# Optimization experiments

Hardware: AMD Instinct MI355X
Metric: run time of the kernel (lower is better)

Reference implementation:

```python
import jax, jax.numpy as jnp
import numpy as np

E = 512   # embed_size
H = 8     # num_heads
D = E // H
N = 4
T = 2048


def quantize(x, b, e):
    # fake-quant: scale by 2^e, clamp to signed b-bit range, floor, dequant
    s = jnp.exp2(e)
    lo = -jnp.exp2(b - 1.0)
    hi = jnp.exp2(b - 1.0) - 1.0
    return jnp.floor(jnp.clip(x / s, lo, hi)) * s


def setup_inputs() -> dict:
    key = jax.random.key(0)
    ks = jax.random.split(key, 8)
    f = lambda k, shape: jax.random.normal(k, shape, dtype=jnp.float32)
    w = 1.0 / np.sqrt(E)  # ~ torch Linear init scale
    return {
        "values": f(ks[0], (N, T, E)),
        "keys": f(ks[1], (N, T, E)),
        "query": f(ks[2], (N, T, E)),
        "Wq": f(ks[3], (E, E)) * w, "bq": jnp.zeros((E,), jnp.float32),
        "Wk": f(ks[4], (E, E)) * w, "bk": jnp.zeros((E,), jnp.float32),
        "Wv": f(ks[5], (E, E)) * w, "bv": jnp.zeros((E,), jnp.float32),
        "Wo": f(ks[6], (E, E)) * w, "bo": jnp.zeros((E,), jnp.float32),
        "b_param": jnp.float32(8.0),
        "e_param": jnp.float32(0.0),
    }


def reference(values, keys, query, Wq, bq, Wk, bk, Wv, bv, Wo, bo, b_param, e_param):
    n, t, emb = query.shape
    d = emb // H
    # linear projections (torch Linear: x @ W^T + b), split heads -> [N,H,T,D]
    q = (query @ Wq.T + bq).reshape(n, t, H, d).transpose(0, 2, 1, 3)
    k = (keys @ Wk.T + bk).reshape(n, t, H, d).transpose(0, 2, 1, 3)
    v = (values @ Wv.T + bv).reshape(n, t, H, d).transpose(0, 2, 1, 3)
    b = jnp.clip(b_param, 1.0, 8.0)
    q = quantize(q, b, e_param)
    k = quantize(k, b, e_param)
    v = quantize(v, b, e_param)
    # NOTE: source scales by sqrt(embed_size), not sqrt(head_dim)
    energy = jnp.einsum('nhqd,nhkd->nhqk', q, k) / jnp.sqrt(jnp.float32(emb))
    attn = jax.nn.softmax(energy, axis=-1)
    out = jnp.einsum('nhqk,nhkd->nhqd', attn, v)
    out = out.transpose(0, 2, 1, 3).reshape(n, t, emb)
    return out @ Wo.T + bo
```

## Files before the change

kernel.cpp:

```cpp
#include <hip/hip_runtime.h>
#include <hip/hip_bf16.h>
#include <hip/hip_fp16.h>
#include <cstdint>
#include <cstddef>


typedef __attribute__((ext_vector_type(8))) _Float16 f16x8;
typedef __attribute__((ext_vector_type(2))) __fp16 hf16x2;
typedef __attribute__((ext_vector_type(16))) float f32x16;
typedef __attribute__((ext_vector_type(4))) unsigned u32x4;
typedef unsigned short u16;

#define EL  4194304
#define WEL 262144

static __device__ __forceinline__ u16 f2h(float x) {
  _Float16 h = (_Float16)x;
  return __builtin_bit_cast(u16, h);
}
static __device__ __forceinline__ unsigned pkh2(float a, float b) {
  hf16x2 p = __builtin_amdgcn_cvt_pkrtz(a, b);
  return __builtin_bit_cast(unsigned, p);
}
static __device__ __forceinline__ void gl_lds16(const void* g, void* l) {
  __builtin_amdgcn_global_load_lds(
      (__attribute__((address_space(1))) void*)g,
      (__attribute__((address_space(3))) void*)l, 16, 0, 0);
}

struct PrepAllArgs { const float* src[7]; };

__global__ __launch_bounds__(256) void prep_all_kernel(PrepAllArgs a,
                                                       u16* __restrict__ dst)
{
  const int i = blockIdx.x * 256 + threadIdx.x;
  const float* src; int off;
  if (i < 3145728) {
    const int m = i >> 20; off = i & 1048575;
    src = (m == 0) ? a.src[0] : (m == 1) ? a.src[1] : a.src[2];
  } else {
    const int j = i - 3145728; const int w = j >> 16; off = j & 65535;
    src = (w == 0) ? a.src[3] : (w == 1) ? a.src[4]
        : (w == 2) ? a.src[5] : a.src[6];
  }
  const float4 v = ((const float4*)src)[off];
  ushort4 o;
  o.x = f2h(v.x); o.y = f2h(v.y); o.z = f2h(v.z); o.w = f2h(v.w);
  ((ushort4*)dst)[i] = o;
}

struct ProjArgs {
  const u16* X[3]; const u16* W[3]; const float* bias[3];
  u16* dst[3]; int trans[3];
};

__global__ __launch_bounds__(256, 3) void proj_kernel(ProjArgs args,
    const float* __restrict__ bparam, const float* __restrict__ eparam)
{
  __shared__ u16 sm[17408];
  u16* const As = sm;
  u16* const Bs = sm + 8192;

  const int z = blockIdx.z;
  const u16* __restrict__ X = args.X[z];
  const u16* __restrict__ W = args.W[z];
  const float* __restrict__ bias = args.bias[z];
  u16* __restrict__ dst = args.dst[z];
  const int mode = args.trans[z];

  const int tid  = threadIdx.x;
  const int lane = tid & 63;
  const int wave = tid >> 6;
  const int lam  = lane & 31;
  const int hl   = lane >> 5;
  const int wm   = wave & 1;
  const int wn   = wave >> 1;
  const int mbase = blockIdx.x * 128;
  const int nbase = blockIdx.y * 128;

  const int srow = tid >> 3;
  const int sj   = (tid & 7) ^ (srow & 7);
  const u16* gA = X + (size_t)(mbase + srow) * 512 + sj * 8;
  const u16* gB = W + (size_t)(nbase + srow) * 512 + sj * 8;

  int offA[2][4], offB[2][4];
#pragma unroll
  for (int f = 0; f < 2; ++f)
#pragma unroll
    for (int kk = 0; kk < 4; ++kk) {
      const int c = 2 * kk + hl;
      const int m = wm * 64 + f * 32 + lam;
      offA[f][kk] = m * 128 + ((c ^ (m & 7)) * 16);
      const int nn = wn * 64 + f * 32 + lam;
      offB[f][kk] = nn * 128 + ((c ^ (nn & 7)) * 16);
    }

  f32x16 acc[2][2];
#pragma unroll
  for (int a = 0; a < 2; ++a)
#pragma unroll
    for (int b = 0; b < 2; ++b)
#pragma unroll
      for (int i = 0; i < 16; ++i) acc[a][b][i] = 0.f;

  for (int kt = 0; kt < 512; kt += 64) {
    __syncthreads();
#pragma unroll
    for (int t = 0; t < 4; ++t) {
      gl_lds16(gA + kt + t * 32 * 512, (char*)As + tid * 16 + t * 4096);
      gl_lds16(gB + kt + t * 32 * 512, (char*)Bs + tid * 16 + t * 4096);
    }
    __syncthreads();

    f16x8 fA[2][4], fB[2][4];
#pragma unroll
    for (int f = 0; f < 2; ++f)
#pragma unroll
      for (int kk = 0; kk < 4; ++kk) {
        fA[f][kk] = *(const f16x8*)((const char*)As + offA[f][kk]);
        fB[f][kk] = *(const f16x8*)((const char*)Bs + offB[f][kk]);
      }
#pragma unroll
    for (int mf = 0; mf < 2; ++mf)
#pragma unroll
      for (int nf = 0; nf < 2; ++nf)
#pragma unroll
        for (int kk = 0; kk < 4; ++kk)
          acc[mf][nf] = __builtin_amdgcn_mfma_f32_32x32x16_f16(
              fA[mf][kk], fB[nf][kk], acc[mf][nf], 0, 0, 0);
  }

  const float bq   = fminf(fmaxf(bparam[0], 1.0f), 8.0f);
  const float e    = eparam[0];
  const float s    = exp2f(e);
  const float invs = exp2f(-e);
  const float qlo  = -exp2f(bq - 1.0f);
  const float qhi  = exp2f(bq - 1.0f) - 1.0f;
  const int nidx = mbase >> 11;
  const int tb   = mbase & 2047;
  const int hb   = nbase >> 6;

  if (mode == 0) {
    const float SCQ = (float)(1.4426950408889634 / 22.627416997969522);
#pragma unroll
    for (int mf = 0; mf < 2; ++mf)
#pragma unroll
      for (int nf = 0; nf < 2; ++nf)
#pragma unroll
        for (int reg = 0; reg < 16; ++reg) {
          int col = wn * 64 + nf * 32 + lam;
          int row = wm * 64 + mf * 32 + (reg & 3) + 8 * (reg >> 2) + 4 * hl;
          float v = acc[mf][nf][reg] + bias[nbase + col];
          float qv = floorf(fminf(fmaxf(v * invs, qlo), qhi)) * s;
          dst[((size_t)(nidx * 8 + hb + (col >> 6)) * 2048 + tb + row) * 64 +
              (col & 63)] = f2h(qv * SCQ);
        }
  } else if (mode == 1) {
#pragma unroll
    for (int mf = 0; mf < 2; ++mf)
#pragma unroll
      for (int nf = 0; nf < 2; ++nf)
#pragma unroll
        for (int reg = 0; reg < 16; ++reg) {
          int col = wn * 64 + nf * 32 + lam;
          int row = wm * 64 + mf * 32 + (reg & 3) + 8 * (reg >> 2) + 4 * hl;
          float v = acc[mf][nf][reg] + bias[nbase + col];
          float qv = floorf(fminf(fmaxf(v * invs, qlo), qhi)) * s;
          const int t = tb + row;
          const int d = col & 63;
          dst[(size_t)(nidx * 8 + hb + (col >> 6)) * 131072 +
              (t >> 5) * 2048 + (t & 31) * 64 + (((d >> 3) ^ (t & 7)) << 3) +
              (d & 7)] = f2h(qv);
        }
  } else {
    __syncthreads();
#pragma unroll
    for (int mf = 0; mf < 2; ++mf)
#pragma unroll
      for (int nf = 0; nf < 2; ++nf)
#pragma unroll
        for (int reg = 0; reg < 16; ++reg) {
          int col = wn * 64 + nf * 32 + lam;
          int row = wm * 64 + mf * 32 + (reg & 3) + 8 * (reg >> 2) + 4 * hl;
          float v = acc[mf][nf][reg] + bias[nbase + col];
          float qv = floorf(fminf(fmaxf(v * invs, qlo), qhi)) * s;
          sm[col * 136 + row] = f2h(qv);
        }
    __syncthreads();
    const int r = tid >> 1, half = tid & 1;
    const u16* sp = sm + r * 136 + half * 64;
    const int d  = r & 63;
    const int sb = d & 1;
    const int rx = (d >> 1) & 7;
    u16* const gp0 = dst + (size_t)(nidx * 8 + hb + (r >> 6)) * 131072 +
                     (d >> 1) * 64;
#pragma unroll
    for (int kb = 0; kb < 2; ++kb) {
      const int Bg = ((tb + half * 64) >> 5) + kb;
#pragma unroll
      for (int g = 0; g < 4; ++g) {
        const int qoff = (g & 1) * 4 + (g >> 1) * 16;
        const uint2 lo = *(const uint2*)(sp + kb * 32 + qoff);
        const uint2 hi = *(const uint2*)(sp + kb * 32 + qoff + 8);
        uint4 val; val.x = lo.x; val.y = lo.y; val.z = hi.x; val.w = hi.y;
        const int s2 = ((g << 1) | sb) ^ rx;
        *(uint4*)(gp0 + Bg * 2048 + s2 * 8) = val;
      }
    }
  }
}

__global__ __launch_bounds__(256, 4) void attn_kernel(
    const u16* __restrict__ qbuf, const u16* __restrict__ kbuf,
    const u16* __restrict__ vtbuf, u16* __restrict__ ctx)
{
  __shared__ u16 sm[17664];
  char* const smc = (char*)sm;

  const int tid  = threadIdx.x;
  const int wave = tid >> 6;
  const int lane = tid & 63;
  const int lam  = lane & 31;
  const int hl   = lane >> 5;
  const int kw   = wave & 1;
  const int qh   = wave >> 1;
  const int bid = blockIdx.x;
  const int wg  = (bid & 7) * 128 + (bid >> 3);
  const int qt = wg & 31;
  const int nh = wg >> 5;
  const int hd = nh & 7;
  const int n  = nh >> 3;
  const int qbase = qt * 64;

  const u16* Qp = qbuf + ((size_t)nh * 2048 + qbase + qh * 32) * 64;
  const u16* gK = kbuf  + (size_t)nh * 131072;
  const u16* gV = vtbuf + (size_t)nh * 131072;

  f16x8 qf[4];
#pragma unroll
  for (int dk = 0; dk < 4; ++dk)
    qf[dk] = *(const f16x8*)(Qp + lam * 64 + dk * 16 + hl * 8);
#pragma unroll
  for (int dk = 0; dk < 4; ++dk)
    asm volatile("" :: "v"(qf[dk]));

  auto stageK = [&](int tn, char* db) {
    const int e = tn * 4096 + tid * 8;
    gl_lds16(gK + e,        db + tid * 16);
    gl_lds16(gK + e + 2048, db + 4096 + tid * 16);
  };
  auto stageV = [&](int tn, char* db) {
    const int e = tn * 4096 + tid * 8;
    gl_lds16(gV + e,        db + tid * 16);
    gl_lds16(gV + e + 2048, db + 4096 + tid * 16);
  };

  int offK[4];
#pragma unroll
  for (int dk = 0; dk < 4; ++dk)
    offK[dk] = kw * 4096 + lam * 128 + (((2 * dk + hl) ^ (lam & 7)) << 4);
  int offV[2][2];
#pragma unroll
  for (int nf = 0; nf < 2; ++nf)
#pragma unroll
    for (int kkl = 0; kkl < 2; ++kkl) {
      const int R = nf * 16 + (lam >> 1);
      const int s2 = (((2 * kkl + hl) << 1) | (lam & 1)) ^ (R & 7);
      offV[nf][kkl] = 16384 + kw * 4096 + R * 128 + s2 * 16;
    }

  f32x16 Zc;
#pragma unroll
  for (int i = 0; i < 16; ++i) Zc[i] = 0.f;

  float l_acc = 0.f;
  f32x16 O[2];
#pragma unroll
  for (int b = 0; b < 2; ++b)
#pragma unroll
    for (int i = 0; i < 16; ++i) O[b][i] = 0.f;

  stageK(0, smc + 8192);
  stageV(0, smc + 16384);
  stageK(1, smc);
  asm volatile("s_waitcnt vmcnt(4)" ::: "memory");
  __builtin_amdgcn_s_barrier();
  f16x8 pf0, pf1;
  {
    f16x8 Kf[4];
#pragma unroll
    for (int dk = 0; dk < 4; ++dk)
      Kf[dk] = *(const f16x8*)(smc + 8192 + offK[dk]);
    f32x16 S;
    S = __builtin_amdgcn_mfma_f32_32x32x16_f16(Kf[0], qf[0], Zc, 0, 0, 0);
    S = __builtin_amdgcn_mfma_f32_32x32x16_f16(Kf[1], qf[1], S, 0, 0, 0);
    S = __builtin_amdgcn_mfma_f32_32x32x16_f16(Kf[2], qf[2], S, 0, 0, 0);
    S = __builtin_amdgcn_mfma_f32_32x32x16_f16(Kf[3], qf[3], S, 0, 0, 0);
    u32x4 fr[2];
#pragma unroll
    for (int gh = 0; gh < 4; ++gh) {
      float p0 = __builtin_amdgcn_exp2f(S[4 * gh + 0]);
      float p1 = __builtin_amdgcn_exp2f(S[4 * gh + 1]);
      float p2 = __builtin_amdgcn_exp2f(S[4 * gh + 2]);
      float p3 = __builtin_amdgcn_exp2f(S[4 * gh + 3]);
      l_acc += (p0 + p1) + (p2 + p3);
      fr[gh >> 1][(gh & 1) * 2 + 0] = pkh2(p0, p1);
      fr[gh >> 1][(gh & 1) * 2 + 1] = pkh2(p2, p3);
    }
    pf0 = __builtin_bit_cast(f16x8, fr[0]);
    pf1 = __builtin_bit_cast(f16x8, fr[1]);
  }

  for (int r = 0; r < 31; ++r) {
    asm volatile("s_waitcnt vmcnt(0)" ::: "memory");
    __builtin_amdgcn_s_barrier();
    __builtin_amdgcn_sched_barrier(0);

    const int pb = (r & 1) << 13;
    const int nb = pb ^ 8192;
    stageK((r + 2) & 31, smc + nb);
    stageV((r + 1) & 31, smc + 16384 + nb);

    f16x8 Vf[2][2];
#pragma unroll
    for (int nf = 0; nf < 2; ++nf)
#pragma unroll
      for (int kkl = 0; kkl < 2; ++kkl)
        Vf[nf][kkl] = *(const f16x8*)(smc + pb + offV[nf][kkl]);
    f16x8 Kf[4];
#pragma unroll
    for (int dk = 0; dk < 4; ++dk)
      Kf[dk] = *(const f16x8*)(smc + pb + offK[dk]);

    __builtin_amdgcn_s_setprio(1);
    O[0] = __builtin_amdgcn_mfma_f32_32x32x16_f16(pf0, Vf[0][0], O[0], 0, 0, 0);
    O[0] = __builtin_amdgcn_mfma_f32_32x32x16_f16(pf1, Vf[0][1], O[0], 0, 0, 0);
    O[1] = __builtin_amdgcn_mfma_f32_32x32x16_f16(pf0, Vf[1][0], O[1], 0, 0, 0);
    O[1] = __builtin_amdgcn_mfma_f32_32x32x16_f16(pf1, Vf[1][1], O[1], 0, 0, 0);
    f32x16 S;
    S = __builtin_amdgcn_mfma_f32_32x32x16_f16(Kf[0], qf[0], Zc, 0, 0, 0);
    S = __builtin_amdgcn_mfma_f32_32x32x16_f16(Kf[1], qf[1], S, 0, 0, 0);
    S = __builtin_amdgcn_mfma_f32_32x32x16_f16(Kf[2], qf[2], S, 0, 0, 0);
    S = __builtin_amdgcn_mfma_f32_32x32x16_f16(Kf[3], qf[3], S, 0, 0, 0);
    __builtin_amdgcn_s_setprio(0);

    u32x4 fr[2];
#pragma unroll
    for (int gh = 0; gh < 4; ++gh) {
      float p0 = __builtin_amdgcn_exp2f(S[4 * gh + 0]);
      float p1 = __builtin_amdgcn_exp2f(S[4 * gh + 1]);
      float p2 = __builtin_amdgcn_exp2f(S[4 * gh + 2]);
      float p3 = __builtin_amdgcn_exp2f(S[4 * gh + 3]);
      l_acc += (p0 + p1) + (p2 + p3);
      fr[gh >> 1][(gh & 1) * 2 + 0] = pkh2(p0, p1);
      fr[gh >> 1][(gh & 1) * 2 + 1] = pkh2(p2, p3);
    }
    pf0 = __builtin_bit_cast(f16x8, fr[0]);
    pf1 = __builtin_bit_cast(f16x8, fr[1]);
  }

  asm volatile("s_waitcnt vmcnt(0)" ::: "memory");
  __builtin_amdgcn_s_barrier();
  {
    f16x8 Vf[2][2];
#pragma unroll
    for (int nf = 0; nf < 2; ++nf)
#pragma unroll
      for (int kkl = 0; kkl < 2; ++kkl)
        Vf[nf][kkl] = *(const f16x8*)(smc + 8192 + offV[nf][kkl]);
    O[0] = __builtin_amdgcn_mfma_f32_32x32x16_f16(pf0, Vf[0][0], O[0], 0, 0, 0);
    O[0] = __builtin_amdgcn_mfma_f32_32x32x16_f16(pf1, Vf[0][1], O[0], 0, 0, 0);
    O[1] = __builtin_amdgcn_mfma_f32_32x32x16_f16(pf0, Vf[1][0], O[1], 0, 0, 0);
    O[1] = __builtin_amdgcn_mfma_f32_32x32x16_f16(pf1, Vf[1][1], O[1], 0, 0, 0);
  }

  l_acc += __shfl_xor(l_acc, 32);
  float* lred = (float*)(smc + 34816);
  if (hl == 0) lred[wave * 32 + lam] = l_acc;
  __syncthreads();

  float* Ow = (float*)(smc + wave * 8704);
#pragma unroll
  for (int nf = 0; nf < 2; ++nf)
#pragma unroll
    for (int r = 0; r < 16; ++r) {
      const int qrow = (r & 3) + 8 * (r >> 2) + 4 * hl;
      Ow[qrow * 68 + nf * 32 + lam] = O[nf][r];
    }
  __syncthreads();

  const int q  = tid >> 2;
  const int dc = (tid & 3) * 16;
  const int qh2 = q >> 5;
  float a[16];
  {
    const char* b0 = smc + (qh2 * 2) * 8704 + (q & 31) * 272 + dc * 4;
    const char* b1 = b0 + 8704;
#pragma unroll
    for (int j = 0; j < 4; ++j) {
      const float4 v0 = *(const float4*)(b0 + j * 16);
      const float4 v1 = *(const float4*)(b1 + j * 16);
      a[4 * j + 0] = v0.x + v1.x; a[4 * j + 1] = v0.y + v1.y;
      a[4 * j + 2] = v0.z + v1.z; a[4 * j + 3] = v0.w + v1.w;
    }
  }
  const float lsum = lred[qh2 * 64 + (q & 31)] + lred[qh2 * 64 + 32 + (q & 31)];
  const float rinv = 1.0f / lsum;
  unsigned outp[8];
#pragma unroll
  for (int i = 0; i < 8; ++i)
    outp[i] = pkh2(a[2 * i] * rinv, a[2 * i + 1] * rinv);
  u16* cp = ctx + ((size_t)n * 2048 + qbase + q) * 512 + hd * 64 + dc;
  *(uint4*)cp       = *(const uint4*)&outp[0];
  *(uint4*)(cp + 8) = *(const uint4*)&outp[4];
}

__global__ __launch_bounds__(256) void outproj_kernel(
    const u16* __restrict__ ctxb, const u16* __restrict__ Wof,
    const float* __restrict__ bias, float* __restrict__ out)
{
  __shared__ u16 sm[12288];
  u16* const As = sm;
  u16* const Bs = sm + 4096;

  const int tid  = threadIdx.x;
  const int lane = tid & 63;
  const int wave = tid >> 6;
  const int lam  = lane & 31;
  const int hl   = lane >> 5;
  const int wm   = wave & 1;
  const int wn   = wave >> 1;
  const int mbase = blockIdx.x * 64;
  const int nbase = blockIdx.y * 128;

  const int srow = tid >> 3;
  const int sj   = (tid & 7) ^ (srow & 7);
  const u16* gA = ctxb + (size_t)(mbase + srow) * 512 + sj * 8;
  const u16* gB = Wof  + (size_t)(nbase + srow) * 512 + sj * 8;

  int offA[4], offB[2][4];
#pragma unroll
  for (int kk = 0; kk < 4; ++kk) {
    const int c = 2 * kk + hl;
    const int m = wm * 32 + lam;
    offA[kk] = m * 128 + ((c ^ (m & 7)) * 16);
#pragma unroll
    for (int f = 0; f < 2; ++f) {
      const int nn = wn * 64 + f * 32 + lam;
      offB[f][kk] = nn * 128 + ((c ^ (nn & 7)) * 16);
    }
  }

  f32x16 acc[2];
#pragma unroll
  for (int a = 0; a < 2; ++a)
#pragma unroll
    for (int i = 0; i < 16; ++i) acc[a][i] = 0.f;

  for (int kt = 0; kt < 512; kt += 64) {
    __syncthreads();
#pragma unroll
    for (int t = 0; t < 2; ++t)
      gl_lds16(gA + kt + t * 32 * 512, (char*)As + tid * 16 + t * 4096);
#pragma unroll
    for (int t = 0; t < 4; ++t)
      gl_lds16(gB + kt + t * 32 * 512, (char*)Bs + tid * 16 + t * 4096);
    __syncthreads();

    f16x8 fA[4], fB[2][4];
#pragma unroll
    for (int kk = 0; kk < 4; ++kk) {
      fA[kk] = *(const f16x8*)((const char*)As + offA[kk]);
#pragma unroll
      for (int f = 0; f < 2; ++f)
        fB[f][kk] = *(const f16x8*)((const char*)Bs + offB[f][kk]);
    }
#pragma unroll
    for (int nf = 0; nf < 2; ++nf)
#pragma unroll
      for (int kk = 0; kk < 4; ++kk)
        acc[nf] = __builtin_amdgcn_mfma_f32_32x32x16_f16(
            fA[kk], fB[nf][kk], acc[nf], 0, 0, 0);
  }

#pragma unroll
  for (int nf = 0; nf < 2; ++nf)
#pragma unroll
    for (int reg = 0; reg < 16; ++reg) {
      int col = nbase + wn * 64 + nf * 32 + lam;
      int row = mbase + wm * 32 + (reg & 3) + 8 * (reg >> 2) + 4 * hl;
      out[(size_t)row * 512 + col] = acc[nf][reg] + bias[col];
    }
}

extern "C" void kernel_launch(void* const* d_in, const int* in_sizes, int n_in,
                              void* d_out, int out_size, void* d_ws, size_t ws_size,
                              hipStream_t stream) {
  (void)in_sizes; (void)n_in; (void)out_size; (void)ws_size;
  const float* values = (const float*)d_in[0];
  const float* keys   = (const float*)d_in[1];
  const float* query  = (const float*)d_in[2];
  const float* Wq = (const float*)d_in[3];  const float* bq = (const float*)d_in[4];
  const float* Wk = (const float*)d_in[5];  const float* bk = (const float*)d_in[6];
  const float* Wv = (const float*)d_in[7];  const float* bv = (const float*)d_in[8];
  const float* Wo = (const float*)d_in[9];  const float* bo = (const float*)d_in[10];
  const float* bp = (const float*)d_in[11]; const float* ep = (const float*)d_in[12];

  u16* ws    = (u16*)d_ws;
  u16* qbuf  = ws;
  u16* kbuf  = ws + (size_t)EL;
  u16* vtbuf = ws + (size_t)2 * EL;
  u16* ctx   = ws + (size_t)3 * EL;
  u16* xwf   = ws + (size_t)4 * EL;

  PrepAllArgs pa;
  pa.src[0] = query; pa.src[1] = keys; pa.src[2] = values;
  pa.src[3] = Wq; pa.src[4] = Wk; pa.src[5] = Wv; pa.src[6] = Wo;
  prep_all_kernel<<<13312, 256, 0, stream>>>(pa, xwf);

  const float* Bsrc[3] = {bq, bk, bv};
  u16* Dst[3] = {qbuf, kbuf, vtbuf};
  ProjArgs a;
  for (int m = 0; m < 3; ++m) {
    a.X[m] = xwf + (size_t)m * EL;
    a.W[m] = xwf + (size_t)3 * EL + (size_t)m * WEL;
    a.bias[m] = Bsrc[m]; a.dst[m] = Dst[m]; a.trans[m] = m;
  }
  proj_kernel<<<dim3(64, 4, 3), 256, 0, stream>>>(a, bp, ep);

  attn_kernel<<<dim3(1024), 256, 0, stream>>>(qbuf, kbuf, vtbuf, ctx);
  outproj_kernel<<<dim3(128, 4), 256, 0, stream>>>(
      ctx, xwf + (size_t)3 * EL + (size_t)3 * WEL, bo, (float*)d_out);
}
```

Baseline: 181.0 us.

## Stage Q/K projection epilogue through LDS and enlarge outproj tile to 128x128

The Q and K projection epilogues now write quantized fp16 results into shared memory first, then emit coalesced 16-byte row stores (with the XOR swizzle applied per 8-element chunk for K). This replaces scattered 2-byte global stores. The output projection kernel doubles its M tile to 128, giving each wave a 2x2 MFMA fragment grid, and sets a launch bound of 3 blocks per CU. The bigger tile improves operand reuse but halves the grid to 256 blocks and raises register and LDS use per block.

```diff
diff --git a/kernel.cpp b/kernel.cpp
--- a/kernel.cpp
+++ b/kernel.cpp
@@ -140,8 +140,10 @@
   const int tb   = mbase & 2047;
   const int hb   = nbase >> 6;
 
-  if (mode == 0) {
-    const float SCQ = (float)(1.4426950408889634 / 22.627416997969522);
+  if (mode != 2) {
+    const float SCQ = (mode == 0)
+        ? (float)(1.4426950408889634 / 22.627416997969522) : 1.0f;
+    __syncthreads();
 #pragma unroll
     for (int mf = 0; mf < 2; ++mf)
 #pragma unroll
@@ -152,26 +154,26 @@
           int row = wm * 64 + mf * 32 + (reg & 3) + 8 * (reg >> 2) + 4 * hl;
           float v = acc[mf][nf][reg] + bias[nbase + col];
           float qv = floorf(fminf(fmaxf(v * invs, qlo), qhi)) * s;
-          dst[((size_t)(nidx * 8 + hb + (col >> 6)) * 2048 + tb + row) * 64 +
-              (col & 63)] = f2h(qv * SCQ);
+          sm[row * 136 + col] = f2h(qv * SCQ);
         }
-  } else if (mode == 1) {
-#pragma unroll
-    for (int mf = 0; mf < 2; ++mf)
-#pragma unroll
-      for (int nf = 0; nf < 2; ++nf)
-#pragma unroll
-        for (int reg = 0; reg < 16; ++reg) {
-          int col = wn * 64 + nf * 32 + lam;
-          int row = wm * 64 + mf * 32 + (reg & 3) + 8 * (reg >> 2) + 4 * hl;
-          float v = acc[mf][nf][reg] + bias[nbase + col];
-          float qv = floorf(fminf(fmaxf(v * invs, qlo), qhi)) * s;
-          const int t = tb + row;
-          const int d = col & 63;
-          dst[(size_t)(nidx * 8 + hb + (col >> 6)) * 131072 +
-              (t >> 5) * 2048 + (t & 31) * 64 + (((d >> 3) ^ (t & 7)) << 3) +
-              (d & 7)] = f2h(qv);
-        }
+    __syncthreads();
+    const int r  = tid & 127;
+    const int hh = tid >> 7;
+    const u16* sp = sm + r * 136 + hh * 64;
+    const int t = tb + r;
+    if (mode == 0) {
+      u16* gp = dst + ((size_t)(nidx * 8 + hb + hh) * 2048 + t) * 64;
+#pragma unroll
+      for (int j = 0; j < 8; ++j)
+        *(uint4*)(gp + j * 8) = *(const uint4*)(sp + j * 8);
+    } else {
+      u16* gp = dst + (size_t)(nidx * 8 + hb + hh) * 131072 +
+                (t >> 5) * 2048 + (t & 31) * 64;
+      const int tx = t & 7;
+#pragma unroll
+      for (int j = 0; j < 8; ++j)
+        *(uint4*)(gp + ((j ^ tx) * 8)) = *(const uint4*)(sp + j * 8);
+    }
   } else {
     __syncthreads();
 #pragma unroll
@@ -415,13 +417,13 @@
   *(uint4*)(cp + 8) = *(const uint4*)&outp[4];
 }
 
-__global__ __launch_bounds__(256) void outproj_kernel(
+__global__ __launch_bounds__(256, 3) void outproj_kernel(
     const u16* __restrict__ ctxb, const u16* __restrict__ Wof,
     const float* __restrict__ bias, float* __restrict__ out)
 {
-  __shared__ u16 sm[12288];
+  __shared__ u16 sm[16384];
   u16* const As = sm;
-  u16* const Bs = sm + 4096;
+  u16* const Bs = sm + 8192;
 
   const int tid  = threadIdx.x;
   const int lane = tid & 63;
@@ -430,7 +432,7 @@
   const int hl   = lane >> 5;
   const int wm   = wave & 1;
   const int wn   = wave >> 1;
-  const int mbase = blockIdx.x * 64;
+  const int mbase = blockIdx.x * 128;
   const int nbase = blockIdx.y * 128;
 
   const int srow = tid >> 3;
@@ -438,59 +440,63 @@
   const u16* gA = ctxb + (size_t)(mbase + srow) * 512 + sj * 8;
   const u16* gB = Wof  + (size_t)(nbase + srow) * 512 + sj * 8;
 
-  int offA[4], offB[2][4];
-#pragma unroll
-  for (int kk = 0; kk < 4; ++kk) {
-    const int c = 2 * kk + hl;
-    const int m = wm * 32 + lam;
-    offA[kk] = m * 128 + ((c ^ (m & 7)) * 16);
-#pragma unroll
-    for (int f = 0; f < 2; ++f) {
+  int offA[2][4], offB[2][4];
+#pragma unroll
+  for (int f = 0; f < 2; ++f)
+#pragma unroll
+    for (int kk = 0; kk < 4; ++kk) {
+      const int c = 2 * kk + hl;
+      const int m = wm * 64 + f * 32 + lam;
+      offA[f][kk] = m * 128 + ((c ^ (m & 7)) * 16);
       const int nn = wn * 64 + f * 32 + lam;
       offB[f][kk] = nn * 128 + ((c ^ (nn & 7)) * 16);
     }
-  }
-
-  f32x16 acc[2];
+
+  f32x16 acc[2][2];
 #pragma unroll
   for (int a = 0; a < 2; ++a)
 #pragma unroll
-    for (int i = 0; i < 16; ++i) acc[a][i] = 0.f;
+    for (int b = 0; b < 2; ++b)
+#pragma unroll
+      for (int i = 0; i < 16; ++i) acc[a][b][i] = 0.f;
 
   for (int kt = 0; kt < 512; kt += 64) {
     __syncthreads();
 #pragma unroll
-    for (int t = 0; t < 2; ++t)
+    for (int t = 0; t < 4; ++t) {
       gl_lds16(gA + kt + t * 32 * 512, (char*)As + tid * 16 + t * 4096);
-#pragma unroll
-    for (int t = 0; t < 4; ++t)
       gl_lds16(gB + kt + t * 32 * 512, (char*)Bs + tid * 16 + t * 4096);
-    __syncthreads();
-
-    f16x8 fA[4], fB[2][4];
-#pragma unroll
-    for (int kk = 0; kk < 4; ++kk) {
-      fA[kk] = *(const f16x8*)((const char*)As + offA[kk]);
-#pragma unroll
-      for (int f = 0; f < 2; ++f)
+    }
+    __syncthreads();
+
+    f16x8 fA[2][4], fB[2][4];
+#pragma unroll
+    for (int f = 0; f < 2; ++f)
+#pragma unroll
+      for (int kk = 0; kk < 4; ++kk) {
+        fA[f][kk] = *(const f16x8*)((const char*)As + offA[f][kk]);
         fB[f][kk] = *(const f16x8*)((const char*)Bs + offB[f][kk]);
-    }
+      }
+#pragma unroll
+    for (int mf = 0; mf < 2; ++mf)
+#pragma unroll
+      for (int nf = 0; nf < 2; ++nf)
+#pragma unroll
+        for (int kk = 0; kk < 4; ++kk)
+          acc[mf][nf] = __builtin_amdgcn_mfma_f32_32x32x16_f16(
+              fA[mf][kk], fB[nf][kk], acc[mf][nf], 0, 0, 0);
+  }
+
+#pragma unroll
+  for (int mf = 0; mf < 2; ++mf)
 #pragma unroll
     for (int nf = 0; nf < 2; ++nf)
 #pragma unroll
-      for (int kk = 0; kk < 4; ++kk)
-        acc[nf] = __builtin_amdgcn_mfma_f32_32x32x16_f16(
-            fA[kk], fB[nf][kk], acc[nf], 0, 0, 0);
-  }
-
-#pragma unroll
-  for (int nf = 0; nf < 2; ++nf)
-#pragma unroll
-    for (int reg = 0; reg < 16; ++reg) {
-      int col = nbase + wn * 64 + nf * 32 + lam;
-      int row = mbase + wm * 32 + (reg & 3) + 8 * (reg >> 2) + 4 * hl;
-      out[(size_t)row * 512 + col] = acc[nf][reg] + bias[col];
-    }
+      for (int reg = 0; reg < 16; ++reg) {
+        int col = nbase + wn * 64 + nf * 32 + lam;
+        int row = mbase + wm * 64 + mf * 32 + (reg & 3) + 8 * (reg >> 2) + 4 * hl;
+        out[(size_t)row * 512 + col] = acc[mf][nf][reg] + bias[col];
+      }
 }
 
 extern "C" void kernel_launch(void* const* d_in, const int* in_sizes, int n_in,
@@ -529,6 +535,6 @@
   proj_kernel<<<dim3(64, 4, 3), 256, 0, stream>>>(a, bp, ep);
 
   attn_kernel<<<dim3(1024), 256, 0, stream>>>(qbuf, kbuf, vtbuf, ctx);
-  outproj_kernel<<<dim3(128, 4), 256, 0, stream>>>(
+  outproj_kernel<<<dim3(64, 4), 256, 0, stream>>>(
       ctx, xwf + (size_t)3 * EL + (size_t)3 * WEL, bo, (float*)d_out);
 }
```

New measurement: 188.7 us. +4.3%, slower.
